# Kernel optimization log

Measured on AMD Instinct MI355X. Metric: run time of the kernel, lower is better.

The kernel has to match this reference:

```python
import jax, jax.numpy as jnp
import numpy as np


def setup_inputs() -> dict:
    key = jax.random.key(0)
    ks = jax.random.split(key, 4)
    B, N, C, S, D_AGG, D_OUT = 16, 2048, 128, 25, 128, 128
    # sparse binary adjacency, avg degree ~ N*0.01 ~ 20
    A = (jax.random.uniform(ks[0], (B, N, N)) < 0.01).astype(jnp.float32)
    X = jax.random.normal(ks[1], (B, N, C), dtype=jnp.float32)
    Wa = jax.random.normal(ks[2], (C, D_AGG), dtype=jnp.float32) * 0.05
    ba = jnp.zeros((D_AGG,), jnp.float32)
    Wc = jax.random.normal(ks[3], (C + D_AGG, D_OUT), dtype=jnp.float32) * 0.05
    bc = jnp.zeros((D_OUT,), jnp.float32)
    return {"A": A, "X": X, "Wa": Wa, "ba": ba, "Wc": Wc, "bc": bc, "n_samples": S}


def reference(A, X, Wa, ba, Wc, bc, n_samples):
    # Per node: take up to n_samples neighbors (nonzero adjacency entries).
    # Original randomly subsamples when degree > S; we take the first S by
    # index (lax.top_k is stable, ties -> lowest index). Missing slots are
    # zero rows, matching the original tf.pad: they contribute relu(ba) to
    # the max-aggregator, exactly like the padded/no-neighbor branches.
    mask = (A != 0).astype(X.dtype)                      # [B,N,N]
    vals, idx = jax.lax.top_k(mask, n_samples)           # [B,N,S]
    feats = jax.vmap(lambda x, i: jnp.take(x, i, axis=0))(X, idx)  # [B,N,S,C]
    feats = feats * vals[..., None]                      # zero padded slots
    # max aggregator: relu(neigh @ Wa + ba), max over sampled neighbors
    h = jax.nn.relu(jnp.einsum('bnsc,cd->bnsd', feats, Wa) + ba)
    agg = h.max(axis=2)                                  # [B,N,D_AGG]
    # concat self features with aggregated, project, relu
    cat = jnp.concatenate([X, agg], axis=-1)             # [B,N,C+D_AGG]
    out = jax.nn.relu(jnp.einsum('bnk,ko->bno', cat, Wc) + bc)  # [B,N,D_OUT]
    # per-graph Frobenius-norm normalization with div_no_nan semantics
    norm = jnp.sqrt(jnp.sum(out * out, axis=(1, 2), keepdims=True))
    return jnp.where(norm > 0, out / norm, jnp.zeros_like(out))
```

## Files before the change

### kernel.cpp

```cpp
#include <hip/hip_runtime.h>


typedef __attribute__((ext_vector_type(8))) short short8;
typedef __attribute__((ext_vector_type(4))) float f32x4;
typedef __attribute__((ext_vector_type(4))) float fvec4;
typedef unsigned int uint;
typedef unsigned short ushort;

__device__ __forceinline__ ushort f2bf(float x) {
    uint u = __builtin_bit_cast(uint, x);
    u += 0x7FFFu + ((u >> 16) & 1u);
    return (ushort)(u >> 16);
}
__device__ __forceinline__ float bflo(uint h) { uint v = h << 16;         return __builtin_bit_cast(float, v); }
__device__ __forceinline__ float bfhi(uint h) { uint v = h & 0xFFFF0000u; return __builtin_bit_cast(float, v); }

__global__ __launch_bounds__(256) void prep_w_k(
    const float* __restrict__ Wa, ushort* __restrict__ Wat)
{
    int i = blockIdx.x * 256 + threadIdx.x;
    int d = i >> 7, k = i & 127;
    Wat[i] = f2bf(Wa[k * 128 + d]);
}

__global__ __launch_bounds__(256) void gemm_mfma_k(
    const float*  __restrict__ Xf,
    const ushort* __restrict__ A1,
    const ushort* __restrict__ Bt,
    const float*  __restrict__ bias,
    ushort* __restrict__ outH,
    float*  __restrict__ outF,
    float*  __restrict__ partials,
    int ktiles)
{
    __shared__ ushort Asm[128 * 128];
    __shared__ ushort Bsm[128 * 128];
    __shared__ float wred[4];
    const int tid = threadIdx.x;
    const int l = tid & 63, w = tid >> 6;
    const int wm = (w >> 1) * 64, wn = (w & 1) * 64;
    const size_t row0 = (size_t)blockIdx.x * 128;
    const int KT = ktiles << 7;

    f32x4 acc[4][4] = {};

    for (int t = 0; t < ktiles; ++t) {
        __syncthreads();
        if (t == 0) {
#pragma unroll
            for (int j = 0; j < 8; ++j) {
                int gid = (j << 8) + tid;
                int r = gid >> 4, g = gid & 15;
                const float* s = Xf + (row0 + r) * 128 + g * 8;
                short8 pk;
#pragma unroll
                for (int e = 0; e < 8; ++e) pk[e] = (short)f2bf(s[e]);
                *(short8*)&Asm[r * 128 + ((g ^ (r & 7)) << 3)] = pk;
            }
        } else {
#pragma unroll
            for (int j = 0; j < 8; ++j) {
                int gid = (j << 8) + tid;
                int r = gid >> 4, g = gid & 15;
                short8 v = *(const short8*)(A1 + (row0 + r) * 128 + g * 8);
                *(short8*)&Asm[r * 128 + ((g ^ (r & 7)) << 3)] = v;
            }
        }
#pragma unroll
        for (int j = 0; j < 8; ++j) {
            int gid = (j << 8) + tid;
            int r = gid >> 4, g = gid & 15;
            short8 v = *(const short8*)(Bt + (size_t)r * KT + (t << 7) + g * 8);
            *(short8*)&Bsm[r * 128 + ((g ^ (r & 7)) << 3)] = v;
        }
        __syncthreads();
#pragma unroll
        for (int ks = 0; ks < 4; ++ks) {
            int gg = (ks << 2) + (l >> 4);
            short8 af[4], bfr[4];
#pragma unroll
            for (int m = 0; m < 4; ++m) {
                int r = wm + m * 16 + (l & 15);
                af[m] = *(const short8*)&Asm[r * 128 + ((gg ^ (r & 7)) << 3)];
            }
#pragma unroll
            for (int n = 0; n < 4; ++n) {
                int c = wn + n * 16 + (l & 15);
                bfr[n] = *(const short8*)&Bsm[c * 128 + ((gg ^ (c & 7)) << 3)];
            }
#pragma unroll
            for (int m = 0; m < 4; ++m)
#pragma unroll
                for (int n = 0; n < 4; ++n)
                    acc[m][n] = __builtin_amdgcn_mfma_f32_16x16x32_bf16(
                        af[m], bfr[n], acc[m][n], 0, 0, 0);
        }
    }

    float bcol[4];
#pragma unroll
    for (int n = 0; n < 4; ++n) bcol[n] = bias[wn + n * 16 + (l & 15)];
    float lsum = 0.f;
#pragma unroll
    for (int m = 0; m < 4; ++m) {
        int rbase = wm + m * 16 + ((l >> 4) << 2);
#pragma unroll
        for (int n = 0; n < 4; ++n) {
            int col = wn + n * 16 + (l & 15);
#pragma unroll
            for (int r = 0; r < 4; ++r) {
                float v = fmaxf(acc[m][n][r] + bcol[n], 0.f);
                size_t o = (row0 + rbase + r) * 128 + col;
                if (outH) outH[o] = f2bf(v);
                else { outF[o] = v; lsum += v * v; }
            }
        }
    }
    if (partials) {
#pragma unroll
        for (int off = 32; off > 0; off >>= 1) lsum += __shfl_down(lsum, off);
        if (l == 0) wred[w] = lsum;
        __syncthreads();
        if (tid == 0) partials[blockIdx.x] = wred[0] + wred[1] + wred[2] + wred[3];
    }
}

__global__ __launch_bounds__(256) void agg_k(
    const float* __restrict__ A,
    const uint*  __restrict__ Hu,
    const float* __restrict__ ba,
    uint* __restrict__ aggu,
    const int* __restrict__ nsp,
    const float* __restrict__ Wc,
    ushort* __restrict__ Wct)
{
    if (blockIdx.x >= 8192) {
        int j = (blockIdx.x - 8192) * 256 + threadIdx.x;
        int d = j >> 8, k = j & 255;
        Wct[j] = f2bf(Wc[k * 128 + d]);
        return;
    }

    __shared__ int idxs[4][32];
    const int l = threadIdx.x & 63;
    const int w = threadIdx.x >> 6;
    const int bid   = blockIdx.x;
    const int xcd   = bid & 7;
    const int grp   = bid >> 3;
    const int batch = ((grp >> 9) << 3) + xcd;
    const int node  = (batch << 11) + ((grp & 511) << 2) + w;
    int S = nsp[0]; if (S > 32) S = 32;

    const fvec4* rowp = (const fvec4*)(A + (size_t)node * 2048);
    fvec4 v[8];
#pragma unroll
    for (int c = 0; c < 8; ++c)
        v[c] = __builtin_nontemporal_load(rowp + c * 64 + l);

    const unsigned long long lt = (1ull << l) - 1ull;
    int base = 0;
#pragma unroll
    for (int c = 0; c < 8; ++c) {
        if (base < S) {
            unsigned long long m0 = __ballot(v[c][0] != 0.f);
            unsigned long long m1 = __ballot(v[c][1] != 0.f);
            unsigned long long m2 = __ballot(v[c][2] != 0.f);
            unsigned long long m3 = __ballot(v[c][3] != 0.f);
            int below = __popcll(m0 & lt) + __popcll(m1 & lt)
                      + __popcll(m2 & lt) + __popcll(m3 & lt);
            int o0 = (int)((m0 >> l) & 1), o1 = (int)((m1 >> l) & 1);
            int o2 = (int)((m2 >> l) & 1), o3 = (int)((m3 >> l) & 1);
            int r0 = base + below;
            int r1 = r0 + o0, r2 = r1 + o1, r3 = r2 + o2;
            int e = (c << 8) + (l << 2);
            if (o0 && r0 < S) idxs[w][r0] = e;
            if (o1 && r1 < S) idxs[w][r1] = e + 1;
            if (o2 && r2 < S) idxs[w][r2] = e + 2;
            if (o3 && r3 < S) idxs[w][r3] = e + 3;
            base += __popcll(m0) + __popcll(m1) + __popcll(m2) + __popcll(m3);
        }
    }
    int found = base < S ? base : S;

    float i0 = fmaxf(ba[2 * l], 0.f), i1 = fmaxf(ba[2 * l + 1], 0.f);
    float r0f = i0, r1f = i1;
    if (found > 0) {
        int fill = idxs[w][0];
        if (l < 32)
            idxs[w][l] = (l < found) ? idxs[w][l] : fill;

        const uint* HB = Hu + ((size_t)batch << 17);
        uint h[32];
#pragma unroll
        for (int q = 0; q < 32; ++q)
            h[q] = HB[(size_t)idxs[w][q] * 64 + l];

        float a0[8], a1[8];
#pragma unroll
        for (int q = 0; q < 8; ++q) { a0[q] = i0; a1[q] = i1; }
#pragma unroll
        for (int q = 0; q < 32; ++q) {
            a0[q & 7] = fmaxf(a0[q & 7], bflo(h[q]));
            a1[q & 7] = fmaxf(a1[q & 7], bfhi(h[q]));
        }
#pragma unroll
        for (int q = 0; q < 4; ++q) {
            a0[q] = fmaxf(a0[q], a0[q + 4]);
            a1[q] = fmaxf(a1[q], a1[q + 4]);
        }
        r0f = fmaxf(fmaxf(a0[0], a0[1]), fmaxf(a0[2], a0[3]));
        r1f = fmaxf(fmaxf(a1[0], a1[1]), fmaxf(a1[2], a1[3]));
    }
    aggu[(size_t)node * 64 + l] = (uint)f2bf(r0f) | ((uint)f2bf(r1f) << 16);
}

__global__ __launch_bounds__(256) void scale_k(
    float* __restrict__ out, const float* __restrict__ partials)
{
    const int blk = blockIdx.x;
    const int b = blk >> 6;
    float s = 0.f;
#pragma unroll
    for (int i = 0; i < 16; ++i) s += partials[b * 16 + i];
    float norm = sqrtf(s);
    float sc = (norm > 0.f) ? (1.f / norm) : 0.f;
    fvec4* o4 = (fvec4*)out;
    int i0 = blk * 1024 + threadIdx.x;
#pragma unroll
    for (int k = 0; k < 4; ++k) {
        fvec4 v = o4[i0 + k * 256];
        o4[i0 + k * 256] = v * sc;
    }
}

extern "C" void kernel_launch(void* const* d_in, const int* in_sizes, int n_in,
                              void* d_out, int out_size, void* d_ws, size_t ws_size,
                              hipStream_t stream) {
    const float* A  = (const float*)d_in[0];
    const float* X  = (const float*)d_in[1];
    const float* Wa = (const float*)d_in[2];
    const float* ba = (const float*)d_in[3];
    const float* Wc = (const float*)d_in[4];
    const float* bc = (const float*)d_in[5];
    const int*  nsp = (const int*)d_in[6];

    float* out = (float*)d_out;
    char* ws = (char*)d_ws;
    ushort* H        = (ushort*)ws;
    ushort* agg      = (ushort*)(ws + (8u << 20));
    ushort* Wat      = (ushort*)(ws + (16u << 20));
    ushort* Wct      = (ushort*)(ws + (16u << 20) + 32768);
    float*  partials = (float*) (ws + (16u << 20) + 131072);

    prep_w_k<<<64, 256, 0, stream>>>(Wa, Wat);
    gemm_mfma_k<<<256, 256, 0, stream>>>(X, nullptr, Wat, ba, H, nullptr, nullptr, 1);
    agg_k<<<8192 + 128, 256, 0, stream>>>(A, (const uint*)H, ba, (uint*)agg, nsp, Wc, Wct);
    gemm_mfma_k<<<256, 256, 0, stream>>>(X, agg, Wct, bc, nullptr, out, partials, 2);
    scale_k<<<1024, 256, 0, stream>>>(out, partials);
}
```

Baseline: 89.04 us.

## Overlap adjacency scan with first GEMM and split gather into separate kernel

Splits the aggregation kernel into a scan that finds up to S neighbor indices per node and a separate gather/max kernel. The scan blocks share one launch with the X·Wa GEMM tiles, so the memory-bound adjacency read runs alongside the MFMA work instead of after it. A sentinel row of relu(ba) is written into H so padded slots need no branch, and weight prep for Wa and Wc is merged into one launch. In exchange, neighbor indices make an extra round trip through global memory, and the scan blocks now allocate the GEMM's full shared-memory footprint, which may lower their occupancy.

```diff
diff --git a/kernel.cpp b/kernel.cpp
--- a/kernel.cpp
+++ b/kernel.cpp
@@ -14,32 +14,43 @@
 }
 __device__ __forceinline__ float bflo(uint h) { uint v = h << 16;         return __builtin_bit_cast(float, v); }
 __device__ __forceinline__ float bfhi(uint h) { uint v = h & 0xFFFF0000u; return __builtin_bit_cast(float, v); }
-
-__global__ __launch_bounds__(256) void prep_w_k(
-    const float* __restrict__ Wa, ushort* __restrict__ Wat)
+__device__ __forceinline__ int mbcnt64(unsigned long long m) {
+    return __builtin_amdgcn_mbcnt_hi((uint)(m >> 32),
+           __builtin_amdgcn_mbcnt_lo((uint)m, 0u));
+}
+
+__global__ __launch_bounds__(256) void prep_k(
+    const float* __restrict__ Wa, const float* __restrict__ Wc,
+    const float* __restrict__ ba,
+    ushort* __restrict__ Wat, ushort* __restrict__ Wct,
+    uint* __restrict__ Hsent)
 {
     int i = blockIdx.x * 256 + threadIdx.x;
-    int d = i >> 7, k = i & 127;
-    Wat[i] = f2bf(Wa[k * 128 + d]);
-}
-
-__global__ __launch_bounds__(256) void gemm_mfma_k(
-    const float*  __restrict__ Xf,
-    const ushort* __restrict__ A1,
-    const ushort* __restrict__ Bt,
-    const float*  __restrict__ bias,
-    ushort* __restrict__ outH,
-    float*  __restrict__ outF,
-    float*  __restrict__ partials,
-    int ktiles)
-{
-    __shared__ ushort Asm[128 * 128];
-    __shared__ ushort Bsm[128 * 128];
-    __shared__ float wred[4];
+    if (i < 16384) {
+        int d = i >> 7, k = i & 127;
+        Wat[i] = f2bf(Wa[k * 128 + d]);
+    } else if (i < 49152) {
+        int j = i - 16384;
+        int d = j >> 8, k = j & 255;
+        Wct[j] = f2bf(Wc[k * 128 + d]);
+    } else if (threadIdx.x < 64) {
+        int t = threadIdx.x;
+        float a = fmaxf(ba[2 * t], 0.f), b = fmaxf(ba[2 * t + 1], 0.f);
+        Hsent[t] = (uint)f2bf(a) | ((uint)f2bf(b) << 16);
+    }
+}
+
+__device__ __forceinline__ void gemm_body(
+    const float*  __restrict__ Xf, const ushort* __restrict__ A1,
+    const ushort* __restrict__ Bt, const float*  __restrict__ bias,
+    ushort* __restrict__ outH, float* __restrict__ outF,
+    float* __restrict__ partials, int ktiles, int tile,
+    ushort* Asm, ushort* Bsm, float* wred)
+{
     const int tid = threadIdx.x;
     const int l = tid & 63, w = tid >> 6;
     const int wm = (w >> 1) * 64, wn = (w & 1) * 64;
-    const size_t row0 = (size_t)blockIdx.x * 128;
+    const size_t row0 = (size_t)tile * 128;
     const int KT = ktiles << 7;
 
     f32x4 acc[4][4] = {};
@@ -121,35 +132,35 @@
         for (int off = 32; off > 0; off >>= 1) lsum += __shfl_down(lsum, off);
         if (l == 0) wred[w] = lsum;
         __syncthreads();
-        if (tid == 0) partials[blockIdx.x] = wred[0] + wred[1] + wred[2] + wred[3];
-    }
-}
-
-__global__ __launch_bounds__(256) void agg_k(
+        if (tid == 0) partials[tile] = wred[0] + wred[1] + wred[2] + wred[3];
+    }
+}
+
+__global__ __launch_bounds__(256) void scanK1_k(
     const float* __restrict__ A,
-    const uint*  __restrict__ Hu,
+    const float* __restrict__ X,
+    const ushort* __restrict__ Wat,
     const float* __restrict__ ba,
-    uint* __restrict__ aggu,
-    const int* __restrict__ nsp,
-    const float* __restrict__ Wc,
-    ushort* __restrict__ Wct)
-{
-    if (blockIdx.x >= 8192) {
-        int j = (blockIdx.x - 8192) * 256 + threadIdx.x;
-        int d = j >> 8, k = j & 255;
-        Wct[j] = f2bf(Wc[k * 128 + d]);
+    ushort* __restrict__ H,
+    ushort* __restrict__ idxg,
+    const int* __restrict__ nsp)
+{
+    __shared__ ushort Asm[128 * 128];
+    __shared__ ushort Bsm[128 * 128];
+    __shared__ float wred[4];
+
+    if (blockIdx.x < 256) {
+        gemm_body(X, nullptr, Wat, ba, H, nullptr, nullptr, 1, blockIdx.x,
+                  Asm, Bsm, wred);
         return;
     }
 
-    __shared__ int idxs[4][32];
+    const int sid = blockIdx.x - 256;
     const int l = threadIdx.x & 63;
     const int w = threadIdx.x >> 6;
-    const int bid   = blockIdx.x;
-    const int xcd   = bid & 7;
-    const int grp   = bid >> 3;
-    const int batch = ((grp >> 9) << 3) + xcd;
-    const int node  = (batch << 11) + ((grp & 511) << 2) + w;
+    const int node = sid * 4 + w;
     int S = nsp[0]; if (S > 32) S = 32;
+    int* idxs = (int*)Bsm;
 
     const fvec4* rowp = (const fvec4*)(A + (size_t)node * 2048);
     fvec4 v[8];
@@ -157,7 +168,7 @@
     for (int c = 0; c < 8; ++c)
         v[c] = __builtin_nontemporal_load(rowp + c * 64 + l);
 
-    const unsigned long long lt = (1ull << l) - 1ull;
+    const int gbase = node & ~2047;
     int base = 0;
 #pragma unroll
     for (int c = 0; c < 8; ++c) {
@@ -166,52 +177,80 @@
             unsigned long long m1 = __ballot(v[c][1] != 0.f);
             unsigned long long m2 = __ballot(v[c][2] != 0.f);
             unsigned long long m3 = __ballot(v[c][3] != 0.f);
-            int below = __popcll(m0 & lt) + __popcll(m1 & lt)
-                      + __popcll(m2 & lt) + __popcll(m3 & lt);
+            int below = mbcnt64(m0) + mbcnt64(m1) + mbcnt64(m2) + mbcnt64(m3);
             int o0 = (int)((m0 >> l) & 1), o1 = (int)((m1 >> l) & 1);
             int o2 = (int)((m2 >> l) & 1), o3 = (int)((m3 >> l) & 1);
             int r0 = base + below;
             int r1 = r0 + o0, r2 = r1 + o1, r3 = r2 + o2;
-            int e = (c << 8) + (l << 2);
-            if (o0 && r0 < S) idxs[w][r0] = e;
-            if (o1 && r1 < S) idxs[w][r1] = e + 1;
-            if (o2 && r2 < S) idxs[w][r2] = e + 2;
-            if (o3 && r3 < S) idxs[w][r3] = e + 3;
+            int e = gbase + (c << 8) + (l << 2);
+            if (o0 && r0 < S) idxs[w * 32 + r0] = e;
+            if (o1 && r1 < S) idxs[w * 32 + r1] = e + 1;
+            if (o2 && r2 < S) idxs[w * 32 + r2] = e + 2;
+            if (o3 && r3 < S) idxs[w * 32 + r3] = e + 3;
             base += __popcll(m0) + __popcll(m1) + __popcll(m2) + __popcll(m3);
         }
     }
     int found = base < S ? base : S;
+    int fill = (found > 0) ? idxs[w * 32] : 32768;
+    if (l < 32) {
+        int val = (l < found) ? idxs[w * 32 + l] : fill;
+        idxg[(size_t)node * 32 + l] = (ushort)val;
+    }
+}
+
+__global__ __launch_bounds__(256) void gather_k(
+    const ushort* __restrict__ idxg,
+    const uint*  __restrict__ Hu,
+    const float* __restrict__ ba,
+    uint* __restrict__ aggu)
+{
+    __shared__ ushort sidx[128];
+    const int l = threadIdx.x & 63;
+    const int w = threadIdx.x >> 6;
+    const int bid = blockIdx.x, xcd = bid & 7, grp = bid >> 3;
+    const int batch = ((grp >> 9) << 3) + xcd;
+    const int node0 = (batch << 11) + ((grp & 511) << 2);
+    const int node = node0 + w;
+
+    if (threadIdx.x < 64)
+        ((uint*)sidx)[threadIdx.x] =
+            ((const uint*)(idxg + (size_t)node0 * 32))[threadIdx.x];
+    __syncthreads();
+
+    uint h[32];
+#pragma unroll
+    for (int q = 0; q < 32; ++q)
+        h[q] = Hu[(size_t)sidx[w * 32 + q] * 64 + l];
 
     float i0 = fmaxf(ba[2 * l], 0.f), i1 = fmaxf(ba[2 * l + 1], 0.f);
-    float r0f = i0, r1f = i1;
-    if (found > 0) {
-        int fill = idxs[w][0];
-        if (l < 32)
-            idxs[w][l] = (l < found) ? idxs[w][l] : fill;
-
-        const uint* HB = Hu + ((size_t)batch << 17);
-        uint h[32];
-#pragma unroll
-        for (int q = 0; q < 32; ++q)
-            h[q] = HB[(size_t)idxs[w][q] * 64 + l];
-
-        float a0[8], a1[8];
-#pragma unroll
-        for (int q = 0; q < 8; ++q) { a0[q] = i0; a1[q] = i1; }
-#pragma unroll
-        for (int q = 0; q < 32; ++q) {
-            a0[q & 7] = fmaxf(a0[q & 7], bflo(h[q]));
-            a1[q & 7] = fmaxf(a1[q & 7], bfhi(h[q]));
-        }
-#pragma unroll
-        for (int q = 0; q < 4; ++q) {
-            a0[q] = fmaxf(a0[q], a0[q + 4]);
-            a1[q] = fmaxf(a1[q], a1[q + 4]);
-        }
-        r0f = fmaxf(fmaxf(a0[0], a0[1]), fmaxf(a0[2], a0[3]));
-        r1f = fmaxf(fmaxf(a1[0], a1[1]), fmaxf(a1[2], a1[3]));
-    }
+    float a0[8], a1[8];
+#pragma unroll
+    for (int q = 0; q < 8; ++q) { a0[q] = i0; a1[q] = i1; }
+#pragma unroll
+    for (int q = 0; q < 32; ++q) {
+        a0[q & 7] = fmaxf(a0[q & 7], bflo(h[q]));
+        a1[q & 7] = fmaxf(a1[q & 7], bfhi(h[q]));
+    }
+#pragma unroll
+    for (int q = 0; q < 4; ++q) {
+        a0[q] = fmaxf(a0[q], a0[q + 4]);
+        a1[q] = fmaxf(a1[q], a1[q + 4]);
+    }
+    float r0f = fmaxf(fmaxf(a0[0], a0[1]), fmaxf(a0[2], a0[3]));
+    float r1f = fmaxf(fmaxf(a1[0], a1[1]), fmaxf(a1[2], a1[3]));
     aggu[(size_t)node * 64 + l] = (uint)f2bf(r0f) | ((uint)f2bf(r1f) << 16);
+}
+
+__global__ __launch_bounds__(256) void gemm_k3_k(
+    const float* __restrict__ X, const ushort* __restrict__ agg,
+    const ushort* __restrict__ Wct, const float* __restrict__ bc,
+    float* __restrict__ out, float* __restrict__ partials)
+{
+    __shared__ ushort Asm[128 * 128];
+    __shared__ ushort Bsm[128 * 128];
+    __shared__ float wred[4];
+    gemm_body(X, agg, Wct, bc, nullptr, out, partials, 2, blockIdx.x,
+              Asm, Bsm, wred);
 }
 
 __global__ __launch_bounds__(256) void scale_k(
@@ -247,14 +286,16 @@
     float* out = (float*)d_out;
     char* ws = (char*)d_ws;
     ushort* H        = (ushort*)ws;
-    ushort* agg      = (ushort*)(ws + (8u << 20));
-    ushort* Wat      = (ushort*)(ws + (16u << 20));
-    ushort* Wct      = (ushort*)(ws + (16u << 20) + 32768);
-    float*  partials = (float*) (ws + (16u << 20) + 131072);
-
-    prep_w_k<<<64, 256, 0, stream>>>(Wa, Wat);
-    gemm_mfma_k<<<256, 256, 0, stream>>>(X, nullptr, Wat, ba, H, nullptr, nullptr, 1);
-    agg_k<<<8192 + 128, 256, 0, stream>>>(A, (const uint*)H, ba, (uint*)agg, nsp, Wc, Wct);
-    gemm_mfma_k<<<256, 256, 0, stream>>>(X, agg, Wct, bc, nullptr, out, partials, 2);
+    ushort* agg      = (ushort*)(ws + (8u << 20) + 4096);
+    ushort* idxg     = (ushort*)(ws + (16u << 20) + 8192);
+    ushort* Wat      = (ushort*)(ws + (18u << 20) + 12288);
+    ushort* Wct      = (ushort*)(ws + (18u << 20) + 12288 + 32768);
+    float*  partials = (float*) (ws + (18u << 20) + 12288 + 98304);
+
+    prep_k<<<193, 256, 0, stream>>>(Wa, Wc, ba, Wat, Wct,
+                                    (uint*)H + (size_t)32768 * 64);
+    scanK1_k<<<8448, 256, 0, stream>>>(A, X, Wat, ba, H, idxg, nsp);
+    gather_k<<<8192, 256, 0, stream>>>(idxg, (const uint*)H, ba, (uint*)agg);
+    gemm_k3_k<<<256, 256, 0, stream>>>(X, agg, Wct, bc, out, partials);
     scale_k<<<1024, 256, 0, stream>>>(out, partials);
 }
```

New measurement: 101.6 us. +14.1%, slower.

## Fuse Frobenius-norm scaling into final GEMM via grid-wide atomic barrier

Applied to the files above, without the earlier changes.

Removes the separate scale kernel by holding the output tile in registers after the final GEMM. Each block publishes its partial sum of squares, waits on a global atomic counter until all 256 blocks have arrived, then scales and writes the output once. This drops one launch and the read-modify-write pass over the output. It relies on all 256 blocks being co-resident (256 blocks fits the device's CUs) and adds a spin-wait barrier.

```diff
diff --git a/kernel.cpp b/kernel.cpp
--- a/kernel.cpp
+++ b/kernel.cpp
@@ -16,33 +16,25 @@
 __device__ __forceinline__ float bfhi(uint h) { uint v = h & 0xFFFF0000u; return __builtin_bit_cast(float, v); }
 
 __global__ __launch_bounds__(256) void prep_w_k(
-    const float* __restrict__ Wa, ushort* __restrict__ Wat)
+    const float* __restrict__ Wa, ushort* __restrict__ Wat,
+    uint* __restrict__ ctr)
 {
     int i = blockIdx.x * 256 + threadIdx.x;
     int d = i >> 7, k = i & 127;
     Wat[i] = f2bf(Wa[k * 128 + d]);
-}
-
-__global__ __launch_bounds__(256) void gemm_mfma_k(
-    const float*  __restrict__ Xf,
-    const ushort* __restrict__ A1,
-    const ushort* __restrict__ Bt,
-    const float*  __restrict__ bias,
-    ushort* __restrict__ outH,
-    float*  __restrict__ outF,
-    float*  __restrict__ partials,
-    int ktiles)
-{
-    __shared__ ushort Asm[128 * 128];
-    __shared__ ushort Bsm[128 * 128];
-    __shared__ float wred[4];
+    if (i == 0) *ctr = 0u;
+}
+
+__device__ __forceinline__ void gemm_core(
+    const float*  __restrict__ Xf, const ushort* __restrict__ A1,
+    const ushort* __restrict__ Bt, int ktiles, int tile,
+    ushort* Asm, ushort* Bsm, f32x4 acc[4][4])
+{
     const int tid = threadIdx.x;
     const int l = tid & 63, w = tid >> 6;
     const int wm = (w >> 1) * 64, wn = (w & 1) * 64;
-    const size_t row0 = (size_t)blockIdx.x * 128;
+    const size_t row0 = (size_t)tile * 128;
     const int KT = ktiles << 7;
-
-    f32x4 acc[4][4] = {};
 
     for (int t = 0; t < ktiles; ++t) {
         __syncthreads();
@@ -96,11 +88,23 @@
                         af[m], bfr[n], acc[m][n], 0, 0, 0);
         }
     }
-
+}
+
+__global__ __launch_bounds__(256) void gemm_k1_k(
+    const float* __restrict__ X, const ushort* __restrict__ Wat,
+    const float* __restrict__ ba, ushort* __restrict__ H)
+{
+    __shared__ ushort Asm[128 * 128];
+    __shared__ ushort Bsm[128 * 128];
+    f32x4 acc[4][4] = {};
+    gemm_core(X, nullptr, Wat, 1, blockIdx.x, Asm, Bsm, acc);
+
+    const int tid = threadIdx.x, l = tid & 63, w = tid >> 6;
+    const int wm = (w >> 1) * 64, wn = (w & 1) * 64;
+    const size_t row0 = (size_t)blockIdx.x * 128;
     float bcol[4];
 #pragma unroll
-    for (int n = 0; n < 4; ++n) bcol[n] = bias[wn + n * 16 + (l & 15)];
-    float lsum = 0.f;
+    for (int n = 0; n < 4; ++n) bcol[n] = ba[wn + n * 16 + (l & 15)];
 #pragma unroll
     for (int m = 0; m < 4; ++m) {
         int rbase = wm + m * 16 + ((l >> 4) << 2);
@@ -110,18 +114,9 @@
 #pragma unroll
             for (int r = 0; r < 4; ++r) {
                 float v = fmaxf(acc[m][n][r] + bcol[n], 0.f);
-                size_t o = (row0 + rbase + r) * 128 + col;
-                if (outH) outH[o] = f2bf(v);
-                else { outF[o] = v; lsum += v * v; }
-            }
-        }
-    }
-    if (partials) {
-#pragma unroll
-        for (int off = 32; off > 0; off >>= 1) lsum += __shfl_down(lsum, off);
-        if (l == 0) wred[w] = lsum;
-        __syncthreads();
-        if (tid == 0) partials[blockIdx.x] = wred[0] + wred[1] + wred[2] + wred[3];
+                H[(row0 + rbase + r) * 128 + col] = f2bf(v);
+            }
+        }
     }
 }
 
@@ -214,22 +209,71 @@
     aggu[(size_t)node * 64 + l] = (uint)f2bf(r0f) | ((uint)f2bf(r1f) << 16);
 }
 
-__global__ __launch_bounds__(256) void scale_k(
-    float* __restrict__ out, const float* __restrict__ partials)
-{
-    const int blk = blockIdx.x;
-    const int b = blk >> 6;
-    float s = 0.f;
-#pragma unroll
-    for (int i = 0; i < 16; ++i) s += partials[b * 16 + i];
-    float norm = sqrtf(s);
-    float sc = (norm > 0.f) ? (1.f / norm) : 0.f;
-    fvec4* o4 = (fvec4*)out;
-    int i0 = blk * 1024 + threadIdx.x;
-#pragma unroll
-    for (int k = 0; k < 4; ++k) {
-        fvec4 v = o4[i0 + k * 256];
-        o4[i0 + k * 256] = v * sc;
+__global__ __launch_bounds__(256) void gemm_k3_k(
+    const float* __restrict__ X, const ushort* __restrict__ agg,
+    const ushort* __restrict__ Wct, const float* __restrict__ bc,
+    float* __restrict__ out, float* __restrict__ partials,
+    uint* __restrict__ ctr)
+{
+    __shared__ ushort Asm[128 * 128];
+    __shared__ ushort Bsm[128 * 128];
+    __shared__ float wred[4];
+    __shared__ float ssc;
+    f32x4 acc[4][4] = {};
+    const int tile = blockIdx.x;
+    gemm_core(X, agg, Wct, 2, tile, Asm, Bsm, acc);
+
+    const int tid = threadIdx.x, l = tid & 63, w = tid >> 6;
+    const int wm = (w >> 1) * 64, wn = (w & 1) * 64;
+    const size_t row0 = (size_t)tile * 128;
+
+    float bcol[4];
+#pragma unroll
+    for (int n = 0; n < 4; ++n) bcol[n] = bc[wn + n * 16 + (l & 15)];
+    float lsum = 0.f;
+#pragma unroll
+    for (int m = 0; m < 4; ++m)
+#pragma unroll
+        for (int n = 0; n < 4; ++n)
+#pragma unroll
+            for (int r = 0; r < 4; ++r) {
+                float v = fmaxf(acc[m][n][r] + bcol[n], 0.f);
+                acc[m][n][r] = v;
+                lsum += v * v;
+            }
+#pragma unroll
+    for (int off = 32; off > 0; off >>= 1) lsum += __shfl_down(lsum, off);
+    if (l == 0) wred[w] = lsum;
+    __syncthreads();
+    if (tid == 0) {
+        partials[tile] = wred[0] + wred[1] + wred[2] + wred[3];
+        __threadfence();
+        __hip_atomic_fetch_add(ctr, 1u, __ATOMIC_ACQ_REL,
+                               __HIP_MEMORY_SCOPE_AGENT);
+        while (__hip_atomic_load(ctr, __ATOMIC_ACQUIRE,
+                                 __HIP_MEMORY_SCOPE_AGENT) < 256u)
+            __builtin_amdgcn_s_sleep(8);
+        float s = 0.f;
+        const int bb = tile >> 4;
+#pragma unroll
+        for (int i = 0; i < 16; ++i)
+            s += __hip_atomic_load(&partials[bb * 16 + i], __ATOMIC_RELAXED,
+                                   __HIP_MEMORY_SCOPE_AGENT);
+        float norm = sqrtf(s);
+        ssc = (norm > 0.f) ? (1.f / norm) : 0.f;
+    }
+    __syncthreads();
+    const float sc = ssc;
+#pragma unroll
+    for (int m = 0; m < 4; ++m) {
+        int rbase = wm + m * 16 + ((l >> 4) << 2);
+#pragma unroll
+        for (int n = 0; n < 4; ++n) {
+            int col = wn + n * 16 + (l & 15);
+#pragma unroll
+            for (int r = 0; r < 4; ++r)
+                out[(row0 + rbase + r) * 128 + col] = acc[m][n][r] * sc;
+        }
     }
 }
 
@@ -251,10 +295,11 @@
     ushort* Wat      = (ushort*)(ws + (16u << 20));
     ushort* Wct      = (ushort*)(ws + (16u << 20) + 32768);
     float*  partials = (float*) (ws + (16u << 20) + 131072);
-
-    prep_w_k<<<64, 256, 0, stream>>>(Wa, Wat);
-    gemm_mfma_k<<<256, 256, 0, stream>>>(X, nullptr, Wat, ba, H, nullptr, nullptr, 1);
-    agg_k<<<8192 + 128, 256, 0, stream>>>(A, (const uint*)H, ba, (uint*)agg, nsp, Wc, Wct);
-    gemm_mfma_k<<<256, 256, 0, stream>>>(X, agg, Wct, bc, nullptr, out, partials, 2);
-    scale_k<<<1024, 256, 0, stream>>>(out, partials);
-}
+    uint*   ctr      = (uint*)  (ws + (16u << 20) + 132096);
+
+    prep_w_k<<<64, 256, 0, stream>>>(Wa, Wat, ctr);
+    gemm_k1_k<<<256, 256, 0, stream>>>(X, Wat, ba, H);
+    agg_k<<<8192 + 128, 256, 0, stream>>>(A, (const uint*)H, ba, (uint*)agg,
+                                          nsp, Wc, Wct);
+    gemm_k3_k<<<256, 256, 0, stream>>>(X, agg, Wct, bc, out, partials, ctr);
+}
```

Measured after the change: 90.68 us. About the same (+1.8%).

## Process two adjacency rows per wave and overlap second scan with first gather

Applied to the files above, without the earlier changes.

The aggregation kernel now assigns two nodes to each wavefront, halving the grid. Both adjacency rows are loaded up front, and the second row's ballot scan is placed between the first row's neighbor gather loads and their max reduction, so index computation overlaps gather latency. The nontemporal load hint on A is dropped and the max reduction uses four accumulators instead of eight. Register pressure rises from two 8-vector row buffers, which may lower occupancy.

```diff
diff --git a/kernel.cpp b/kernel.cpp
--- a/kernel.cpp
+++ b/kernel.cpp
@@ -125,39 +125,9 @@
     }
 }
 
-__global__ __launch_bounds__(256) void agg_k(
-    const float* __restrict__ A,
-    const uint*  __restrict__ Hu,
-    const float* __restrict__ ba,
-    uint* __restrict__ aggu,
-    const int* __restrict__ nsp,
-    const float* __restrict__ Wc,
-    ushort* __restrict__ Wct)
-{
-    if (blockIdx.x >= 8192) {
-        int j = (blockIdx.x - 8192) * 256 + threadIdx.x;
-        int d = j >> 8, k = j & 255;
-        Wct[j] = f2bf(Wc[k * 128 + d]);
-        return;
-    }
-
-    __shared__ int idxs[4][32];
-    const int l = threadIdx.x & 63;
-    const int w = threadIdx.x >> 6;
-    const int bid   = blockIdx.x;
-    const int xcd   = bid & 7;
-    const int grp   = bid >> 3;
-    const int batch = ((grp >> 9) << 3) + xcd;
-    const int node  = (batch << 11) + ((grp & 511) << 2) + w;
-    int S = nsp[0]; if (S > 32) S = 32;
-
-    const fvec4* rowp = (const fvec4*)(A + (size_t)node * 2048);
-    fvec4 v[8];
-#pragma unroll
-    for (int c = 0; c < 8; ++c)
-        v[c] = __builtin_nontemporal_load(rowp + c * 64 + l);
-
-    const unsigned long long lt = (1ull << l) - 1ull;
+__device__ __forceinline__ int scan_row(
+    const fvec4 v[8], int S, unsigned long long lt, int l, int* idx)
+{
     int base = 0;
 #pragma unroll
     for (int c = 0; c < 8; ++c) {
@@ -173,45 +143,102 @@
             int r0 = base + below;
             int r1 = r0 + o0, r2 = r1 + o1, r3 = r2 + o2;
             int e = (c << 8) + (l << 2);
-            if (o0 && r0 < S) idxs[w][r0] = e;
-            if (o1 && r1 < S) idxs[w][r1] = e + 1;
-            if (o2 && r2 < S) idxs[w][r2] = e + 2;
-            if (o3 && r3 < S) idxs[w][r3] = e + 3;
+            if (o0 && r0 < S) idx[r0] = e;
+            if (o1 && r1 < S) idx[r1] = e + 1;
+            if (o2 && r2 < S) idx[r2] = e + 2;
+            if (o3 && r3 < S) idx[r3] = e + 3;
             base += __popcll(m0) + __popcll(m1) + __popcll(m2) + __popcll(m3);
         }
     }
-    int found = base < S ? base : S;
-
-    float i0 = fmaxf(ba[2 * l], 0.f), i1 = fmaxf(ba[2 * l + 1], 0.f);
-    float r0f = i0, r1f = i1;
-    if (found > 0) {
-        int fill = idxs[w][0];
+    return base < S ? base : S;
+}
+
+__device__ __forceinline__ uint gather_max(
+    const uint* HB, const int* idx, int l, float i0, float i1, const uint h[32])
+{
+    float a0[4] = {i0, i0, i0, i0}, a1[4] = {i1, i1, i1, i1};
+#pragma unroll
+    for (int q = 0; q < 32; ++q) {
+        a0[q & 3] = fmaxf(a0[q & 3], bflo(h[q]));
+        a1[q & 3] = fmaxf(a1[q & 3], bfhi(h[q]));
+    }
+    float r0 = fmaxf(fmaxf(a0[0], a0[1]), fmaxf(a0[2], a0[3]));
+    float r1 = fmaxf(fmaxf(a1[0], a1[1]), fmaxf(a1[2], a1[3]));
+    return (uint)f2bf(r0) | ((uint)f2bf(r1) << 16);
+}
+
+__global__ __launch_bounds__(256) void agg_k(
+    const float* __restrict__ A,
+    const uint*  __restrict__ Hu,
+    const float* __restrict__ ba,
+    uint* __restrict__ aggu,
+    const int* __restrict__ nsp,
+    const float* __restrict__ Wc,
+    ushort* __restrict__ Wct)
+{
+    if (blockIdx.x >= 4096) {
+        int j = (blockIdx.x - 4096) * 256 + threadIdx.x;
+        int d = j >> 8, k = j & 255;
+        Wct[j] = f2bf(Wc[k * 128 + d]);
+        return;
+    }
+
+    __shared__ int idxs[4][2][32];
+    const int l = threadIdx.x & 63;
+    const int w = threadIdx.x >> 6;
+    const int bid   = blockIdx.x;
+    const int xcd   = bid & 7;
+    const int grp   = bid >> 3;
+    const int batch = ((grp >> 8) << 3) + xcd;
+    const int nb    = (batch << 11) + ((grp & 255) << 3);
+    const int node0 = nb + 2 * w;
+    const int node1 = node0 + 1;
+    int S = nsp[0]; if (S > 32) S = 32;
+    const unsigned long long lt = (1ull << l) - 1ull;
+    const uint* HB = Hu + ((size_t)batch << 17);
+
+    fvec4 v0[8], v1[8];
+    {
+        const fvec4* r0 = (const fvec4*)(A + (size_t)node0 * 2048);
+        const fvec4* r1 = (const fvec4*)(A + (size_t)node1 * 2048);
+#pragma unroll
+        for (int c = 0; c < 8; ++c) v0[c] = r0[c * 64 + l];
+#pragma unroll
+        for (int c = 0; c < 8; ++c) v1[c] = r1[c * 64 + l];
+    }
+
+    const float i0 = fmaxf(ba[2 * l], 0.f), i1 = fmaxf(ba[2 * l + 1], 0.f);
+
+    int f0 = scan_row(v0, S, lt, l, idxs[w][0]);
+    const bool have0 = f0 > 0;
+
+    uint h[32];
+    if (have0) {
+        int fill = idxs[w][0][0];
         if (l < 32)
-            idxs[w][l] = (l < found) ? idxs[w][l] : fill;
-
-        const uint* HB = Hu + ((size_t)batch << 17);
-        uint h[32];
+            idxs[w][0][l] = (l < f0) ? idxs[w][0][l] : fill;
 #pragma unroll
         for (int q = 0; q < 32; ++q)
-            h[q] = HB[(size_t)idxs[w][q] * 64 + l];
-
-        float a0[8], a1[8];
-#pragma unroll
-        for (int q = 0; q < 8; ++q) { a0[q] = i0; a1[q] = i1; }
-#pragma unroll
-        for (int q = 0; q < 32; ++q) {
-            a0[q & 7] = fmaxf(a0[q & 7], bflo(h[q]));
-            a1[q & 7] = fmaxf(a1[q & 7], bfhi(h[q]));
-        }
-#pragma unroll
-        for (int q = 0; q < 4; ++q) {
-            a0[q] = fmaxf(a0[q], a0[q + 4]);
-            a1[q] = fmaxf(a1[q], a1[q + 4]);
-        }
-        r0f = fmaxf(fmaxf(a0[0], a0[1]), fmaxf(a0[2], a0[3]));
-        r1f = fmaxf(fmaxf(a1[0], a1[1]), fmaxf(a1[2], a1[3]));
-    }
-    aggu[(size_t)node * 64 + l] = (uint)f2bf(r0f) | ((uint)f2bf(r1f) << 16);
+            h[q] = HB[(size_t)idxs[w][0][q] * 64 + l];
+    }
+
+    int f1 = scan_row(v1, S, lt, l, idxs[w][1]);
+
+    uint pack0 = (uint)f2bf(i0) | ((uint)f2bf(i1) << 16);
+    if (have0) pack0 = gather_max(HB, idxs[w][0], l, i0, i1, h);
+    aggu[(size_t)node0 * 64 + l] = pack0;
+
+    uint pack1 = (uint)f2bf(i0) | ((uint)f2bf(i1) << 16);
+    if (f1 > 0) {
+        int fill = idxs[w][1][0];
+        if (l < 32)
+            idxs[w][1][l] = (l < f1) ? idxs[w][1][l] : fill;
+#pragma unroll
+        for (int q = 0; q < 32; ++q)
+            h[q] = HB[(size_t)idxs[w][1][q] * 64 + l];
+        pack1 = gather_max(HB, idxs[w][1], l, i0, i1, h);
+    }
+    aggu[(size_t)node1 * 64 + l] = pack1;
 }
 
 __global__ __launch_bounds__(256) void scale_k(
@@ -254,7 +281,8 @@
 
     prep_w_k<<<64, 256, 0, stream>>>(Wa, Wat);
     gemm_mfma_k<<<256, 256, 0, stream>>>(X, nullptr, Wat, ba, H, nullptr, nullptr, 1);
-    agg_k<<<8192 + 128, 256, 0, stream>>>(A, (const uint*)H, ba, (uint*)agg, nsp, Wc, Wct);
+    agg_k<<<4096 + 128, 256, 0, stream>>>(A, (const uint*)H, ba, (uint*)agg,
+                                          nsp, Wc, Wct);
     gemm_mfma_k<<<256, 256, 0, stream>>>(X, agg, Wct, bc, nullptr, out, partials, 2);
     scale_k<<<1024, 256, 0, stream>>>(out, partials);
 }
```

Result: slower. 97.63 us (+9.6%).
